# Kernel optimization log

Hardware: AMD Instinct MI355X
Metric: run time of the kernel (lower is better)

Reference implementation:

```python
import jax, jax.numpy as jnp
import numpy as np
import math

B, S, D = 4, 2048, 1024

def setup_inputs() -> dict:
    key = jax.random.key(0)
    k_x, k_q, k_k, k_v = jax.random.split(key, 4)
    scale = 1.0 / math.sqrt(D)
    return {
        "x": jax.random.normal(k_x, (B, S, D), dtype=jnp.float32),
        "W_Q": jax.random.normal(k_q, (D, D), dtype=jnp.float32) * scale,
        "W_K": jax.random.normal(k_k, (D, D), dtype=jnp.float32) * scale,
        "W_V": jax.random.normal(k_v, (D, D), dtype=jnp.float32) * scale,
    }

def reference(x, W_Q, W_K, W_V):
    # nn.Linear(bias=False): y = x @ W.T
    Q = jnp.einsum('bsd,ed->bse', x, W_Q)
    K = jnp.einsum('bsd,ed->bse', x, W_K)
    V = jnp.einsum('bsd,ed->bse', x, W_V)
    scores = jnp.einsum('bqd,bkd->bqk', Q, K) / jnp.sqrt(jnp.asarray(Q.shape[-1], Q.dtype))
    weight = jax.nn.softmax(scores, axis=-1)  # [B,S,S]
    return jnp.einsum('bqk,bkd->bqd', weight, V)
```

## Files before the change

kernel.cpp:

```cpp
#include <hip/hip_runtime.h>
#include <stdint.h>

typedef __bf16 bf16;
typedef __bf16 bf16x8 __attribute__((ext_vector_type(8)));
typedef __bf16 bf16x4 __attribute__((ext_vector_type(4)));
typedef float f32x4 __attribute__((ext_vector_type(4)));

__device__ inline void gload_lds16(const void* g, void* l) {
  __builtin_amdgcn_global_load_lds(
      (__attribute__((address_space(1))) void*)g,
      (__attribute__((address_space(3))) void*)l, 16, 0, 0);
}

__global__ __launch_bounds__(256) void cvt_all(
    const float* __restrict__ x, const float* __restrict__ wq,
    const float* __restrict__ wk, const float* __restrict__ wv,
    bf16* __restrict__ xb, bf16* __restrict__ Wb) {
  const int NX = 2097152;
  const int NW = 262144;
  int i = blockIdx.x * 256 + threadIdx.x;
  const int stride = gridDim.x * 256;
  for (int p = i; p < NX + 3 * NW; p += stride) {
    const float* src; bf16* dst; int off;
    if (p < NX) { src = x; dst = xb; off = p; }
    else {
      int q = p - NX; int w = q >> 18; off = q & (NW - 1);
      src = (w == 0) ? wq : ((w == 1) ? wk : wv);
      dst = Wb + (long)w * 1048576;
    }
    float4 v = ((const float4*)src)[off];
    bf16x4 o;
    o[0] = (bf16)v.x; o[1] = (bf16)v.y; o[2] = (bf16)v.z; o[3] = (bf16)v.w;
    ((bf16x4*)dst)[off] = o;
  }
}

template <int MODE>
__global__ __launch_bounds__(512, 2) void gemm8(
    const bf16* __restrict__ Ag, const bf16* __restrict__ Bg,
    void* __restrict__ Cg,
    long lda, long ldb, long ldc,
    long sA, long sB, long sC, int K, float scale)
{
  constexpr int BUFSZ = 65536;
  __shared__ alignas(16) char lds[2 * BUFSZ];
  const int tid = threadIdx.x;
  const int l = tid & 63;
  const int wv = tid >> 6;
  const int fr = l & 15;
  const int kch = l >> 4;
  const int m0 = blockIdx.y * 256;
  const int n0 = blockIdx.x * 256;
  const bf16* Ab = Ag + (long)blockIdx.z * sA;
  const bf16* Bb = Bg + (long)blockIdx.z * sB;

  const int wm = wv >> 2;
  const int wn = wv & 3;

  const int a_rd = fr * 128 + (((wm * 4 + kch) ^ (fr & 7)) << 4);
  const int b_rd = (wn & 1) * 8192 + fr * 128 + ((((wn >> 1) * 4 + kch) ^ (fr & 7)) << 4);

  const int se = (tid & 7) ^ ((tid >> 3) & 7);
  const int s_row = (se >> 2) * 128 + (tid >> 3);
  const int s_k = (se & 3) * 8;
  const int wb16 = (tid & 448) * 16;

  const int NT = K >> 6;
  f32x4 acc[8][4] = {};

  auto stageA = [&](int tile, int kh, int buf) {
#pragma unroll
    for (int rd = 0; rd < 2; ++rd)
      gload_lds16(Ab + (long)(m0 + s_row + rd * 64) * lda + tile * 64 + kh * 32 + s_k,
                  lds + buf * BUFSZ + kh * 16384 + rd * 8192 + wb16);
  };
  auto stageB = [&](int tile, int kh, int buf) {
#pragma unroll
    for (int rd = 0; rd < 2; ++rd)
      gload_lds16(Bb + (long)(n0 + s_row + rd * 64) * ldb + tile * 64 + kh * 32 + s_k,
                  lds + buf * BUFSZ + 32768 + kh * 16384 + rd * 8192 + wb16);
  };

  stageA(0, 0, 0); stageB(0, 0, 0); stageA(0, 1, 0); stageB(0, 1, 0);
  stageA(min(1, NT - 1), 0, 1); stageB(min(1, NT - 1), 0, 1);
  asm volatile("s_waitcnt vmcnt(4)" ::: "memory");
  __builtin_amdgcn_sched_barrier(0);
  __builtin_amdgcn_s_barrier();

  for (int t = 0; t < NT; ++t) {
    const char* bufA = lds + (t & 1) * BUFSZ;
    const char* bufB = bufA + 32768;
    const int t1 = min(t + 1, NT - 1);
    const int t2 = min(t + 2, NT - 1);
    const int nb = (t & 1) ^ 1;
    const int cur = t & 1;

    bf16x8 bfg[4], af[4];
    stageA(t1, 1, nb);
#pragma unroll
    for (int n = 0; n < 4; ++n) bfg[n] = *(const bf16x8*)(bufB + n * 2048 + b_rd);
#pragma unroll
    for (int m = 0; m < 4; ++m) af[m] = *(const bf16x8*)(bufA + m * 2048 + a_rd);
    __builtin_amdgcn_s_barrier();
    __builtin_amdgcn_s_setprio(1);
#pragma unroll
    for (int m = 0; m < 4; ++m)
#pragma unroll
      for (int n = 0; n < 4; ++n)
        acc[m][n] = __builtin_amdgcn_mfma_f32_16x16x32_bf16(af[m], bfg[n], acc[m][n], 0, 0, 0);
    __builtin_amdgcn_s_setprio(0);
    __builtin_amdgcn_s_barrier();
    stageB(t1, 1, nb);
#pragma unroll
    for (int m = 0; m < 4; ++m) af[m] = *(const bf16x8*)(bufA + 8192 + m * 2048 + a_rd);
    __builtin_amdgcn_s_barrier();
    __builtin_amdgcn_s_setprio(1);
#pragma unroll
    for (int m = 0; m < 4; ++m)
#pragma unroll
      for (int n = 0; n < 4; ++n)
        acc[4 + m][n] = __builtin_amdgcn_mfma_f32_16x16x32_bf16(af[m], bfg[n], acc[4 + m][n], 0, 0, 0);
    __builtin_amdgcn_s_setprio(0);
    __builtin_amdgcn_s_barrier();
    stageA(t2, 0, cur);
#pragma unroll
    for (int n = 0; n < 4; ++n) bfg[n] = *(const bf16x8*)(bufB + 16384 + n * 2048 + b_rd);
#pragma unroll
    for (int m = 0; m < 4; ++m) af[m] = *(const bf16x8*)(bufA + 16384 + m * 2048 + a_rd);
    __builtin_amdgcn_s_barrier();
    __builtin_amdgcn_s_setprio(1);
#pragma unroll
    for (int m = 0; m < 4; ++m)
#pragma unroll
      for (int n = 0; n < 4; ++n)
        acc[m][n] = __builtin_amdgcn_mfma_f32_16x16x32_bf16(af[m], bfg[n], acc[m][n], 0, 0, 0);
    __builtin_amdgcn_s_setprio(0);
    __builtin_amdgcn_s_barrier();
    stageB(t2, 0, cur);
#pragma unroll
    for (int m = 0; m < 4; ++m) af[m] = *(const bf16x8*)(bufA + 16384 + 8192 + m * 2048 + a_rd);
    __builtin_amdgcn_s_barrier();
    __builtin_amdgcn_s_setprio(1);
#pragma unroll
    for (int m = 0; m < 4; ++m)
#pragma unroll
      for (int n = 0; n < 4; ++n)
        acc[4 + m][n] = __builtin_amdgcn_mfma_f32_16x16x32_bf16(af[m], bfg[n], acc[4 + m][n], 0, 0, 0);
    __builtin_amdgcn_s_setprio(0);
    asm volatile("s_waitcnt vmcnt(4)" ::: "memory");
    __builtin_amdgcn_sched_barrier(0);
    __builtin_amdgcn_s_barrier();
  }
  asm volatile("s_waitcnt vmcnt(0)" ::: "memory");

#pragma unroll
  for (int mf = 0; mf < 8; ++mf) {
    const int row = m0 + wm * 128 + (mf >> 2) * 64 + (mf & 3) * 16 + (l >> 4) * 4;
#pragma unroll
    for (int n = 0; n < 4; ++n) {
      const int col = n0 + wn * 64 + n * 16 + fr;
      bf16* C = (bf16*)Cg + (long)blockIdx.z * sC;
#pragma unroll
      for (int r = 0; r < 4; ++r)
        C[(long)(row + r) * ldc + col] = (bf16)(acc[mf][n][r] * scale);
    }
  }
}

template <int MODE>
__global__ __launch_bounds__(256, 2) void gemm2h(
    const bf16* __restrict__ Ag, const bf16* __restrict__ Bg,
    void* __restrict__ Cg, void* __restrict__ C2g,
    long lda, long ldb, long ldc,
    long sA, long sB, long sC, int K, float scale)
{
  constexpr int BUFSZ = 32768;
  __shared__ alignas(16) char lds[2 * BUFSZ];
  const int tid = threadIdx.x;
  const int l = tid & 63;
  const int wv = tid >> 6;
  const int wm = wv >> 1, wn = wv & 1;
  const int fr = l & 15;
  const int kch = l >> 4;
  const int m0 = blockIdx.y * 128;
  const int n0 = blockIdx.x * 128;
  const bf16* Ab = Ag + (long)blockIdx.z * sA;
  const bf16* Bb = Bg + (long)blockIdx.z * sB;

  const int a_rd = fr * 128 + (((wm * 4 + kch) ^ (fr & 7)) << 4);
  const int b_rd = fr * 128 + (((wn * 4 + kch) ^ (fr & 7)) << 4);

  const int se = (tid & 7) ^ ((tid >> 3) & 7);
  const int s_row = (se >> 2) * 64 + (tid >> 3);
  const int s_k = (se & 3) * 8;
  const int wb16 = (tid >> 6) * 1024;

  const int NT = K >> 6;
  f32x4 acc[4][4] = {};

  auto stageA = [&](int tile, int kh, int buf) {
#pragma unroll
    for (int rd = 0; rd < 2; ++rd)
      gload_lds16(Ab + (long)(m0 + s_row + rd * 32) * lda + tile * 64 + kh * 32 + s_k,
                  lds + buf * BUFSZ + kh * 8192 + rd * 4096 + wb16);
  };
  auto stageB = [&](int tile, int kh, int buf) {
#pragma unroll
    for (int rd = 0; rd < 2; ++rd)
      gload_lds16(Bb + (long)(n0 + s_row + rd * 32) * ldb + tile * 64 + kh * 32 + s_k,
                  lds + buf * BUFSZ + 16384 + kh * 8192 + rd * 4096 + wb16);
  };

  stageA(0, 0, 0); stageB(0, 0, 0); stageA(0, 1, 0); stageB(0, 1, 0);
  stageA(min(1, NT - 1), 0, 1); stageB(min(1, NT - 1), 0, 1);
  asm volatile("s_waitcnt vmcnt(4)" ::: "memory");
  __builtin_amdgcn_sched_barrier(0);
  __builtin_amdgcn_s_barrier();

  for (int t = 0; t < NT; ++t) {
    const char* bufA = lds + (t & 1) * BUFSZ;
    const char* bufB = bufA + 16384;
    const int t1 = min(t + 1, NT - 1);
    const int t2 = min(t + 2, NT - 1);
    const int nb = (t & 1) ^ 1;
    const int cur = t & 1;

    bf16x8 bfg[4], af[4];
    stageA(t1, 1, nb); stageB(t1, 1, nb);
#pragma unroll
    for (int n = 0; n < 4; ++n) bfg[n] = *(const bf16x8*)(bufB + n * 2048 + b_rd);
#pragma unroll
    for (int m = 0; m < 4; ++m) af[m] = *(const bf16x8*)(bufA + m * 2048 + a_rd);
    __builtin_amdgcn_s_barrier();
    __builtin_amdgcn_s_setprio(1);
#pragma unroll
    for (int m = 0; m < 4; ++m)
#pragma unroll
      for (int n = 0; n < 4; ++n)
        acc[m][n] = __builtin_amdgcn_mfma_f32_16x16x32_bf16(af[m], bfg[n], acc[m][n], 0, 0, 0);
    __builtin_amdgcn_s_setprio(0);
    __builtin_amdgcn_s_barrier();
    stageA(t2, 0, cur); stageB(t2, 0, cur);
#pragma unroll
    for (int n = 0; n < 4; ++n) bfg[n] = *(const bf16x8*)(bufB + 8192 + n * 2048 + b_rd);
#pragma unroll
    for (int m = 0; m < 4; ++m) af[m] = *(const bf16x8*)(bufA + 8192 + m * 2048 + a_rd);
    __builtin_amdgcn_s_barrier();
    __builtin_amdgcn_s_setprio(1);
#pragma unroll
    for (int m = 0; m < 4; ++m)
#pragma unroll
      for (int n = 0; n < 4; ++n)
        acc[m][n] = __builtin_amdgcn_mfma_f32_16x16x32_bf16(af[m], bfg[n], acc[m][n], 0, 0, 0);
    __builtin_amdgcn_s_setprio(0);
    asm volatile("s_waitcnt vmcnt(4)" ::: "memory");
    __builtin_amdgcn_sched_barrier(0);
    __builtin_amdgcn_s_barrier();
  }
  asm volatile("s_waitcnt vmcnt(0)" ::: "memory");

#pragma unroll
  for (int mf = 0; mf < 4; ++mf) {
    const int row = m0 + wm * 64 + mf * 16 + (l >> 4) * 4;
#pragma unroll
    for (int n = 0; n < 4; ++n) {
      const int col = n0 + wn * 64 + n * 16 + fr;
      if constexpr (MODE == 0) {
        if (col < 2048) {
          bf16* C = (bf16*)Cg;
#pragma unroll
          for (int r = 0; r < 4; ++r)
            C[(long)(row + r) * 2048 + col] = (bf16)acc[mf][n][r];
        } else {
          bf16* Vt = (bf16*)C2g;
          const int d = col - 2048;
          const int b = row >> 11;
          const int s = row & 2047;
          bf16x4 pk;
#pragma unroll
          for (int r = 0; r < 4; ++r) pk[r] = (bf16)acc[mf][n][r];
          *(bf16x4*)(Vt + (long)b * 2097152 + (long)d * 2048 + s) = pk;
        }
      } else {
        float* C = (float*)Cg + (long)blockIdx.z * sC;
#pragma unroll
        for (int r = 0; r < 4; ++r)
          C[(long)(row + r) * ldc + col] = acc[mf][n][r] * scale;
      }
    }
  }
}

__global__ __launch_bounds__(256) void softmax_k(const bf16* __restrict__ Sm,
                                                 bf16* __restrict__ P, int cols) {
  __shared__ float red[8];
  const long row = blockIdx.x;
  const bf16* sr = Sm + row * (long)cols;
  bf16* pr = P + row * (long)cols;
  const int t = threadIdx.x;
  bf16x8 v = *(const bf16x8*)(sr + t * 8);
  float e[8];
#pragma unroll
  for (int j = 0; j < 8; ++j) e[j] = (float)v[j];
  float m = e[0];
#pragma unroll
  for (int j = 1; j < 8; ++j) m = fmaxf(m, e[j]);
#pragma unroll
  for (int o = 32; o; o >>= 1) m = fmaxf(m, __shfl_xor(m, o));
  if ((t & 63) == 0) red[t >> 6] = m;
  __syncthreads();
  m = fmaxf(fmaxf(red[0], red[1]), fmaxf(red[2], red[3]));
  float s = 0.f;
#pragma unroll
  for (int j = 0; j < 8; ++j) { e[j] = __expf(e[j] - m); s += e[j]; }
#pragma unroll
  for (int o = 32; o; o >>= 1) s += __shfl_xor(s, o);
  if ((t & 63) == 0) red[4 + (t >> 6)] = s;
  __syncthreads();
  s = red[4] + red[5] + red[6] + red[7];
  const float inv = 1.0f / s;
  bf16x8 o8;
#pragma unroll
  for (int j = 0; j < 8; ++j) o8[j] = (bf16)(e[j] * inv);
  *(bf16x8*)(pr + t * 8) = o8;
}

extern "C" void kernel_launch(void* const* d_in, const int* in_sizes, int n_in,
                              void* d_out, int out_size, void* d_ws, size_t ws_size,
                              hipStream_t stream) {
  const float* x  = (const float*)d_in[0];
  const float* Wq = (const float*)d_in[1];
  const float* Wk = (const float*)d_in[2];
  const float* Wv = (const float*)d_in[3];
  float* out = (float*)d_out;

  char* ws = (char*)d_ws;
  bf16* QKbuf = (bf16*)(ws);
  bf16* P     = (bf16*)(ws);
  bf16* Vt    = (bf16*)(ws + 33554432);
  bf16* scb   = (bf16*)(ws + 50331648);
  bf16* xb    = (bf16*)(ws + 50331648);
  bf16* Wb    = (bf16*)(ws + 67108864);

  dim3 b256(256, 1, 1), b512(512, 1, 1);

  cvt_all<<<2048, b256, 0, stream>>>(x, Wq, Wk, Wv, xb, Wb);

  gemm2h<0><<<dim3(24, 64, 1), b256, 0, stream>>>(
      xb, Wb, QKbuf, Vt, 1024, 1024, 2048, 0, 0, 0, 1024, 1.f);

  gemm8<2><<<dim3(8, 8, 4), b512, 0, stream>>>(
      QKbuf, QKbuf + 1024, scb, 2048, 2048, 2048,
      4194304, 4194304, 4194304, 1024, 0.03125f);

  softmax_k<<<8192, b256, 0, stream>>>(scb, P, 2048);

  gemm2h<1><<<dim3(8, 16, 4), b256, 0, stream>>>(
      P, Vt, out, nullptr, 2048, 2048, 1024,
      4194304, 2097152, 2097152, 2048, 1.f);
}
```

Before: 183.9 us.

## Enlarge GEMM tile to 256x128 with four-phase interleaved LDS staging

The 128x128 GEMM kernel used for the QKV projection and the P·V product is replaced by a 256x128 tile. Each warp now computes 128x64 with 8x4 accumulators, and each B fragment is reused across two A sub-tiles. A and B staging is interleaved across four MFMA phases per K tile, with the vmcnt waits adjusted to match. This raises arithmetic intensity and cuts B reloads, at the cost of one block per CU (96KB LDS, launch bounds 1) and fewer blocks: 768 for the projection and 256 for P·V on a device with roughly 256 CUs.

```diff
diff --git a/kernel.cpp b/kernel.cpp
--- a/kernel.cpp
+++ b/kernel.cpp
@@ -168,13 +168,13 @@
 }
 
 template <int MODE>
-__global__ __launch_bounds__(256, 2) void gemm2h(
+__global__ __launch_bounds__(256, 1) void gemm4(
     const bf16* __restrict__ Ag, const bf16* __restrict__ Bg,
     void* __restrict__ Cg, void* __restrict__ C2g,
     long lda, long ldb, long ldc,
     long sA, long sB, long sC, int K, float scale)
 {
-  constexpr int BUFSZ = 32768;
+  constexpr int BUFSZ = 49152;
   __shared__ alignas(16) char lds[2 * BUFSZ];
   const int tid = threadIdx.x;
   const int l = tid & 63;
@@ -182,7 +182,7 @@
   const int wm = wv >> 1, wn = wv & 1;
   const int fr = l & 15;
   const int kch = l >> 4;
-  const int m0 = blockIdx.y * 128;
+  const int m0 = blockIdx.y * 256;
   const int n0 = blockIdx.x * 128;
   const bf16* Ab = Ag + (long)blockIdx.z * sA;
   const bf16* Bb = Bg + (long)blockIdx.z * sB;
@@ -191,42 +191,43 @@
   const int b_rd = fr * 128 + (((wn * 4 + kch) ^ (fr & 7)) << 4);
 
   const int se = (tid & 7) ^ ((tid >> 3) & 7);
-  const int s_row = (se >> 2) * 64 + (tid >> 3);
+  const int s_rowA = (se >> 2) * 128 + (tid >> 3);
+  const int s_rowB = (se >> 2) * 64 + (tid >> 3);
   const int s_k = (se & 3) * 8;
   const int wb16 = (tid >> 6) * 1024;
 
   const int NT = K >> 6;
-  f32x4 acc[4][4] = {};
+  f32x4 acc[8][4] = {};
 
   auto stageA = [&](int tile, int kh, int buf) {
 #pragma unroll
-    for (int rd = 0; rd < 2; ++rd)
-      gload_lds16(Ab + (long)(m0 + s_row + rd * 32) * lda + tile * 64 + kh * 32 + s_k,
-                  lds + buf * BUFSZ + kh * 8192 + rd * 4096 + wb16);
+    for (int rd = 0; rd < 4; ++rd)
+      gload_lds16(Ab + (long)(m0 + s_rowA + rd * 32) * lda + tile * 64 + kh * 32 + s_k,
+                  lds + buf * BUFSZ + kh * 16384 + rd * 4096 + wb16);
   };
   auto stageB = [&](int tile, int kh, int buf) {
 #pragma unroll
     for (int rd = 0; rd < 2; ++rd)
-      gload_lds16(Bb + (long)(n0 + s_row + rd * 32) * ldb + tile * 64 + kh * 32 + s_k,
-                  lds + buf * BUFSZ + 16384 + kh * 8192 + rd * 4096 + wb16);
+      gload_lds16(Bb + (long)(n0 + s_rowB + rd * 32) * ldb + tile * 64 + kh * 32 + s_k,
+                  lds + buf * BUFSZ + 32768 + kh * 8192 + rd * 4096 + wb16);
   };
 
   stageA(0, 0, 0); stageB(0, 0, 0); stageA(0, 1, 0); stageB(0, 1, 0);
   stageA(min(1, NT - 1), 0, 1); stageB(min(1, NT - 1), 0, 1);
-  asm volatile("s_waitcnt vmcnt(4)" ::: "memory");
+  asm volatile("s_waitcnt vmcnt(6)" ::: "memory");
   __builtin_amdgcn_sched_barrier(0);
   __builtin_amdgcn_s_barrier();
 
   for (int t = 0; t < NT; ++t) {
     const char* bufA = lds + (t & 1) * BUFSZ;
-    const char* bufB = bufA + 16384;
+    const char* bufB = bufA + 32768;
     const int t1 = min(t + 1, NT - 1);
     const int t2 = min(t + 2, NT - 1);
     const int nb = (t & 1) ^ 1;
     const int cur = t & 1;
 
     bf16x8 bfg[4], af[4];
-    stageA(t1, 1, nb); stageB(t1, 1, nb);
+    stageA(t1, 1, nb);
 #pragma unroll
     for (int n = 0; n < 4; ++n) bfg[n] = *(const bf16x8*)(bufB + n * 2048 + b_rd);
 #pragma unroll
@@ -240,11 +241,23 @@
         acc[m][n] = __builtin_amdgcn_mfma_f32_16x16x32_bf16(af[m], bfg[n], acc[m][n], 0, 0, 0);
     __builtin_amdgcn_s_setprio(0);
     __builtin_amdgcn_s_barrier();
-    stageA(t2, 0, cur); stageB(t2, 0, cur);
+    stageB(t1, 1, nb);
+#pragma unroll
+    for (int m = 0; m < 4; ++m) af[m] = *(const bf16x8*)(bufA + 8192 + m * 2048 + a_rd);
+    __builtin_amdgcn_s_barrier();
+    __builtin_amdgcn_s_setprio(1);
+#pragma unroll
+    for (int m = 0; m < 4; ++m)
+#pragma unroll
+      for (int n = 0; n < 4; ++n)
+        acc[4 + m][n] = __builtin_amdgcn_mfma_f32_16x16x32_bf16(af[m], bfg[n], acc[4 + m][n], 0, 0, 0);
+    __builtin_amdgcn_s_setprio(0);
+    __builtin_amdgcn_s_barrier();
+    stageA(t2, 0, cur);
 #pragma unroll
     for (int n = 0; n < 4; ++n) bfg[n] = *(const bf16x8*)(bufB + 8192 + n * 2048 + b_rd);
 #pragma unroll
-    for (int m = 0; m < 4; ++m) af[m] = *(const bf16x8*)(bufA + 8192 + m * 2048 + a_rd);
+    for (int m = 0; m < 4; ++m) af[m] = *(const bf16x8*)(bufA + 16384 + m * 2048 + a_rd);
     __builtin_amdgcn_s_barrier();
     __builtin_amdgcn_s_setprio(1);
 #pragma unroll
@@ -253,15 +266,27 @@
       for (int n = 0; n < 4; ++n)
         acc[m][n] = __builtin_amdgcn_mfma_f32_16x16x32_bf16(af[m], bfg[n], acc[m][n], 0, 0, 0);
     __builtin_amdgcn_s_setprio(0);
-    asm volatile("s_waitcnt vmcnt(4)" ::: "memory");
+    __builtin_amdgcn_s_barrier();
+    stageB(t2, 0, cur);
+#pragma unroll
+    for (int m = 0; m < 4; ++m) af[m] = *(const bf16x8*)(bufA + 16384 + 8192 + m * 2048 + a_rd);
+    __builtin_amdgcn_s_barrier();
+    __builtin_amdgcn_s_setprio(1);
+#pragma unroll
+    for (int m = 0; m < 4; ++m)
+#pragma unroll
+      for (int n = 0; n < 4; ++n)
+        acc[4 + m][n] = __builtin_amdgcn_mfma_f32_16x16x32_bf16(af[m], bfg[n], acc[4 + m][n], 0, 0, 0);
+    __builtin_amdgcn_s_setprio(0);
+    asm volatile("s_waitcnt vmcnt(6)" ::: "memory");
     __builtin_amdgcn_sched_barrier(0);
     __builtin_amdgcn_s_barrier();
   }
   asm volatile("s_waitcnt vmcnt(0)" ::: "memory");
 
 #pragma unroll
-  for (int mf = 0; mf < 4; ++mf) {
-    const int row = m0 + wm * 64 + mf * 16 + (l >> 4) * 4;
+  for (int mf = 0; mf < 8; ++mf) {
+    const int row = m0 + wm * 128 + (mf >> 2) * 64 + (mf & 3) * 16 + (l >> 4) * 4;
 #pragma unroll
     for (int n = 0; n < 4; ++n) {
       const int col = n0 + wn * 64 + n * 16 + fr;
@@ -346,7 +371,7 @@
 
   cvt_all<<<2048, b256, 0, stream>>>(x, Wq, Wk, Wv, xb, Wb);
 
-  gemm2h<0><<<dim3(24, 64, 1), b256, 0, stream>>>(
+  gemm4<0><<<dim3(24, 32, 1), b256, 0, stream>>>(
       xb, Wb, QKbuf, Vt, 1024, 1024, 2048, 0, 0, 0, 1024, 1.f);
 
   gemm8<2><<<dim3(8, 8, 4), b512, 0, stream>>>(
@@ -355,7 +380,7 @@
 
   softmax_k<<<8192, b256, 0, stream>>>(scb, P, 2048);
 
-  gemm2h<1><<<dim3(8, 16, 4), b256, 0, stream>>>(
+  gemm4<1><<<dim3(8, 8, 4), b256, 0, stream>>>(
       P, Vt, out, nullptr, 2048, 2048, 1024,
       4194304, 2097152, 2097152, 2048, 1.f);
 }
```

Result: slower. 210.2 us (+14.3%).

## Compute QKV projection transposed with larger 384x256 tiles in dedicated kernel

Applied to the files above, without the earlier changes.

Replaces the 128x128-tile QKV projection with a new 512-thread kernel that computes W·xᵀ using 384x256 output tiles, three A sub-tiles per K step and double-buffered LDS. Swapping operands makes the V output contiguous along the sequence, so Vt is written directly, while Q/K are written as packed 4-element column stores. The larger tile is meant to raise arithmetic intensity and cut global reload traffic and launch count for the projection. The cost is 192 accumulator registers per thread, which may pressure occupancy, plus scattered scalar Vt stores and uncoalesced Q/K writes. The remaining GEMM templates are simplified to drop unused modes.

```diff
diff --git a/kernel.cpp b/kernel.cpp
--- a/kernel.cpp
+++ b/kernel.cpp
@@ -35,10 +35,125 @@
   }
 }
 
-template <int MODE>
+__global__ __launch_bounds__(512, 2) void projT(
+    const bf16* __restrict__ Wg, const bf16* __restrict__ Xg,
+    bf16* __restrict__ QKbuf, bf16* __restrict__ Vt)
+{
+  constexpr int BUFSZ = 40960;
+  __shared__ alignas(16) char lds[2 * BUFSZ];
+  const int tid = threadIdx.x;
+  const int l = tid & 63;
+  const int wv = tid >> 6;
+  const int wm = wv >> 2;
+  const int wn = wv & 3;
+  const int fr = l & 15;
+  const int kch = l >> 4;
+  const int m0 = blockIdx.y * 384;
+  const int n0 = blockIdx.x * 256;
+
+  const int a_rd = fr * 128 + (((wm * 4 + kch) ^ (fr & 7)) << 4);
+  const int b_rd = 24576 + (wn & 1) * 8192 + fr * 128 + ((((wn >> 1) * 4 + kch) ^ (fr & 7)) << 4);
+
+  const int se = (tid & 7) ^ ((tid >> 3) & 7);
+  const int s_rowA = (se >> 2) * 192 + (tid >> 3);
+  const int s_rowB = (se >> 2) * 128 + (tid >> 3);
+  const int s_k = (se & 3) * 8;
+  const int wb16 = (tid & 448) * 16;
+
+  const int NT = 32;
+  f32x4 acc[12][4] = {};
+
+  auto stageA = [&](int tile, int buf, int rd) {
+    gload_lds16(Wg + (long)(m0 + s_rowA + rd * 64) * 1024 + tile * 32 + s_k,
+                lds + buf * BUFSZ + rd * 8192 + wb16);
+  };
+  auto stageB = [&](int tile, int buf, int rd) {
+    gload_lds16(Xg + (long)(n0 + s_rowB + rd * 64) * 1024 + tile * 32 + s_k,
+                lds + buf * BUFSZ + 24576 + rd * 8192 + wb16);
+  };
+
+  stageA(0, 0, 0); stageB(0, 0, 0); stageA(0, 0, 1); stageB(0, 0, 1); stageA(0, 0, 2);
+  stageA(1, 1, 0); stageB(1, 1, 0); stageA(1, 1, 1);
+  asm volatile("s_waitcnt vmcnt(3)" ::: "memory");
+  __builtin_amdgcn_sched_barrier(0);
+  __builtin_amdgcn_s_barrier();
+
+  for (int t = 0; t < NT; ++t) {
+    const char* buf = lds + (t & 1) * BUFSZ;
+    const int t1 = min(t + 1, NT - 1);
+    const int t2 = min(t + 2, NT - 1);
+    const int nb = (t & 1) ^ 1;
+    const int cur = t & 1;
+
+    bf16x8 bfg[4], af[4];
+    stageA(t1, nb, 2); stageB(t1, nb, 1);
+#pragma unroll
+    for (int n = 0; n < 4; ++n) bfg[n] = *(const bf16x8*)(buf + n * 2048 + b_rd);
+#pragma unroll
+    for (int m = 0; m < 4; ++m) af[m] = *(const bf16x8*)(buf + m * 2048 + a_rd);
+    __builtin_amdgcn_s_barrier();
+    __builtin_amdgcn_s_setprio(1);
+#pragma unroll
+    for (int m = 0; m < 4; ++m)
+#pragma unroll
+      for (int n = 0; n < 4; ++n)
+        acc[m][n] = __builtin_amdgcn_mfma_f32_16x16x32_bf16(af[m], bfg[n], acc[m][n], 0, 0, 0);
+    __builtin_amdgcn_s_setprio(0);
+    __builtin_amdgcn_s_barrier();
+    stageA(t2, cur, 0); stageB(t2, cur, 0);
+#pragma unroll
+    for (int m = 0; m < 4; ++m) af[m] = *(const bf16x8*)(buf + 8192 + m * 2048 + a_rd);
+    __builtin_amdgcn_s_barrier();
+    __builtin_amdgcn_s_setprio(1);
+#pragma unroll
+    for (int m = 0; m < 4; ++m)
+#pragma unroll
+      for (int n = 0; n < 4; ++n)
+        acc[4 + m][n] = __builtin_amdgcn_mfma_f32_16x16x32_bf16(af[m], bfg[n], acc[4 + m][n], 0, 0, 0);
+    __builtin_amdgcn_s_setprio(0);
+    __builtin_amdgcn_s_barrier();
+    stageA(t2, cur, 1);
+#pragma unroll
+    for (int m = 0; m < 4; ++m) af[m] = *(const bf16x8*)(buf + 16384 + m * 2048 + a_rd);
+    __builtin_amdgcn_s_barrier();
+    __builtin_amdgcn_s_setprio(1);
+#pragma unroll
+    for (int m = 0; m < 4; ++m)
+#pragma unroll
+      for (int n = 0; n < 4; ++n)
+        acc[8 + m][n] = __builtin_amdgcn_mfma_f32_16x16x32_bf16(af[m], bfg[n], acc[8 + m][n], 0, 0, 0);
+    __builtin_amdgcn_s_setprio(0);
+    asm volatile("s_waitcnt vmcnt(3)" ::: "memory");
+    __builtin_amdgcn_sched_barrier(0);
+    __builtin_amdgcn_s_barrier();
+  }
+  asm volatile("s_waitcnt vmcnt(0)" ::: "memory");
+
+#pragma unroll
+  for (int mf = 0; mf < 12; ++mf) {
+    const int wrow = m0 + wm * 192 + (mf >> 2) * 64 + (mf & 3) * 16 + (l >> 4) * 4;
+#pragma unroll
+    for (int n = 0; n < 4; ++n) {
+      const int xrow = n0 + wn * 64 + n * 16 + fr;
+      if (wrow < 2048) {
+        bf16x4 pk;
+#pragma unroll
+        for (int r = 0; r < 4; ++r) pk[r] = (bf16)acc[mf][n][r];
+        *(bf16x4*)(QKbuf + (long)xrow * 2048 + wrow) = pk;
+      } else {
+        const int b = xrow >> 11;
+        const int s = xrow & 2047;
+#pragma unroll
+        for (int r = 0; r < 4; ++r)
+          Vt[(long)b * 2097152 + (long)(wrow - 2048 + r) * 2048 + s] = (bf16)acc[mf][n][r];
+      }
+    }
+  }
+}
+
 __global__ __launch_bounds__(512, 2) void gemm8(
     const bf16* __restrict__ Ag, const bf16* __restrict__ Bg,
-    void* __restrict__ Cg,
+    bf16* __restrict__ Cg,
     long lda, long ldb, long ldc,
     long sA, long sB, long sC, int K, float scale)
 {
@@ -159,7 +274,7 @@
 #pragma unroll
     for (int n = 0; n < 4; ++n) {
       const int col = n0 + wn * 64 + n * 16 + fr;
-      bf16* C = (bf16*)Cg + (long)blockIdx.z * sC;
+      bf16* C = Cg + (long)blockIdx.z * sC;
 #pragma unroll
       for (int r = 0; r < 4; ++r)
         C[(long)(row + r) * ldc + col] = (bf16)(acc[mf][n][r] * scale);
@@ -167,12 +282,11 @@
   }
 }
 
-template <int MODE>
 __global__ __launch_bounds__(256, 2) void gemm2h(
     const bf16* __restrict__ Ag, const bf16* __restrict__ Bg,
-    void* __restrict__ Cg, void* __restrict__ C2g,
+    float* __restrict__ Cg,
     long lda, long ldb, long ldc,
-    long sA, long sB, long sC, int K, float scale)
+    long sA, long sB, long sC, int K)
 {
   constexpr int BUFSZ = 32768;
   __shared__ alignas(16) char lds[2 * BUFSZ];
@@ -265,28 +379,10 @@
 #pragma unroll
     for (int n = 0; n < 4; ++n) {
       const int col = n0 + wn * 64 + n * 16 + fr;
-      if constexpr (MODE == 0) {
-        if (col < 2048) {
-          bf16* C = (bf16*)Cg;
-#pragma unroll
-          for (int r = 0; r < 4; ++r)
-            C[(long)(row + r) * 2048 + col] = (bf16)acc[mf][n][r];
-        } else {
-          bf16* Vt = (bf16*)C2g;
-          const int d = col - 2048;
-          const int b = row >> 11;
-          const int s = row & 2047;
-          bf16x4 pk;
-#pragma unroll
-          for (int r = 0; r < 4; ++r) pk[r] = (bf16)acc[mf][n][r];
-          *(bf16x4*)(Vt + (long)b * 2097152 + (long)d * 2048 + s) = pk;
-        }
-      } else {
-        float* C = (float*)Cg + (long)blockIdx.z * sC;
-#pragma unroll
-        for (int r = 0; r < 4; ++r)
-          C[(long)(row + r) * ldc + col] = acc[mf][n][r] * scale;
-      }
+      float* C = Cg + (long)blockIdx.z * sC;
+#pragma unroll
+      for (int r = 0; r < 4; ++r)
+        C[(long)(row + r) * ldc + col] = acc[mf][n][r];
     }
   }
 }
@@ -346,16 +442,15 @@
 
   cvt_all<<<2048, b256, 0, stream>>>(x, Wq, Wk, Wv, xb, Wb);
 
-  gemm2h<0><<<dim3(24, 64, 1), b256, 0, stream>>>(
-      xb, Wb, QKbuf, Vt, 1024, 1024, 2048, 0, 0, 0, 1024, 1.f);
-
-  gemm8<2><<<dim3(8, 8, 4), b512, 0, stream>>>(
+  projT<<<dim3(32, 8, 1), b512, 0, stream>>>(Wb, xb, QKbuf, Vt);
+
+  gemm8<<<dim3(8, 8, 4), b512, 0, stream>>>(
       QKbuf, QKbuf + 1024, scb, 2048, 2048, 2048,
       4194304, 4194304, 4194304, 1024, 0.03125f);
 
   softmax_k<<<8192, b256, 0, stream>>>(scb, P, 2048);
 
-  gemm2h<1><<<dim3(8, 16, 4), b256, 0, stream>>>(
-      P, Vt, out, nullptr, 2048, 2048, 1024,
-      4194304, 2097152, 2097152, 2048, 1.f);
-}
+  gemm2h<<<dim3(8, 16, 4), b256, 0, stream>>>(
+      P, Vt, out, 2048, 2048, 1024,
+      4194304, 2097152, 2097152, 2048);
+}
```

After: 167.6 us. -8.9%, faster.
